# Kernel tuning notes

Measured on AMD Instinct MI355X. Metric: run time of the kernel, lower is better.

Reference implementation:

```python
import jax, jax.numpy as jnp
import numpy as np

N, D_IN, D_OUT, E, K = 32768, 1024, 1024, 8, 2
LN_EPS = 1e-5


def setup_inputs() -> dict:
    key = jax.random.key(0)
    ks = jax.random.split(key, 7)
    x = jax.random.normal(ks[0], (N, D_IN), dtype=jnp.float32)
    # gate: Linear(D_IN, E) then Tanh
    Wg = jax.random.normal(ks[1], (D_IN, E), dtype=jnp.float32) * 0.02
    bg = jnp.zeros((E,), dtype=jnp.float32)
    # experts: stacked Linear(D_IN, D_OUT) weights, [E, D_IN, D_OUT]
    We = jax.random.normal(ks[2], (E, D_IN, D_OUT), dtype=jnp.float32) * 0.02
    be = jnp.zeros((E, D_OUT), dtype=jnp.float32)
    # per-expert LayerNorm params
    gamma = jnp.ones((E, D_OUT), dtype=jnp.float32)
    beta = jnp.zeros((E, D_OUT), dtype=jnp.float32)
    return {"x": x, "Wg": Wg, "bg": bg, "We": We, "be": be,
            "gamma": gamma, "beta": beta}


def reference(x, Wg, bg, We, be, gamma, beta):
    # gating: Linear + Tanh, then top-k over experts, softmax over the k gates
    gate_logits = jnp.tanh(x @ Wg + bg)                      # [N, E]
    top_g, top_i = jax.lax.top_k(gate_logits, K)             # [N, K], [N, K]
    gates = jax.nn.softmax(top_g, axis=-1)                   # [N, K]

    # all experts computed densely (faithful to original): Linear + GELU + LN
    h = jnp.einsum('ni,eio->neo', x, We) + be[None]          # [N, E, D_OUT]
    h = jax.nn.gelu(h, approximate=False)                    # torch nn.GELU (exact)
    mu = jnp.mean(h, axis=-1, keepdims=True)
    var = jnp.mean(jnp.square(h - mu), axis=-1, keepdims=True)
    h = (h - mu) * jax.lax.rsqrt(var + LN_EPS)
    h = h * gamma[None] + beta[None]                         # [N, E, D_OUT]

    # gather top-k expert outputs and combine with softmax gates
    sel = jnp.take_along_axis(h, top_i[:, :, None], axis=1)  # [N, K, D_OUT]
    return jnp.sum(sel * gates[:, :, None], axis=1)          # [N, D_OUT]
```

## Files before the change

kernel.cpp:

```cpp
#include <hip/hip_runtime.h>
#include <hip/hip_bf16.h>

#define N_TOK 32768
#define D_IN 1024
#define D_OUT 1024
#define NE 8

#define BM 128
#define BN 128
#define BK 64
#define PAD 72

#define GBLK 64
#define GCH 64
#define NCH (D_IN / GCH)
#define CNT_STRIDE 64

#define AS1 __attribute__((address_space(1)))
#define AS3 __attribute__((address_space(3)))

typedef __attribute__((ext_vector_type(8))) short short8;
typedef __attribute__((ext_vector_type(4))) float floatx4;

__device__ __forceinline__ unsigned short f2bf(float f) {
    union { float f; unsigned u; } v; v.f = f;
    unsigned r = v.u + 0x7fffu + ((v.u >> 16) & 1u);
    return (unsigned short)(r >> 16);
}
__device__ __forceinline__ float bf2f(unsigned short u) {
    union { unsigned u; float f; } v; v.u = ((unsigned)u) << 16;
    return v.f;
}

__device__ __forceinline__ void gl_lds16(const void* g, void* l) {
    __builtin_amdgcn_global_load_lds((const AS1 unsigned int*)g,
                                     (AS3 unsigned int*)l, 16, 0, 0);
}

__global__ void zero_cnt(int* __restrict__ cnt) {
    int i = blockIdx.x * 256 + threadIdx.x;
    if (i < 16 * CNT_STRIDE) cnt[i] = 0;
}

__global__ __launch_bounds__(256) void transpose_we(
    const float* __restrict__ We, unsigned short* __restrict__ WeT)
{
    __shared__ unsigned short tile[64 * 65];
    int e = blockIdx.z;
    int i0 = blockIdx.x * 64, o0 = blockIdx.y * 64;
    const float* src = We + ((size_t)e * D_IN + i0) * D_OUT + o0;
#pragma unroll
    for (int it = 0; it < 16; ++it) {
        int idx = threadIdx.x + it * 256;
        int r = idx >> 6, c = idx & 63;
        tile[r * 65 + c] = f2bf(src[(size_t)r * D_OUT + c]);
    }
    __syncthreads();
    unsigned short* dst = WeT + ((size_t)e * D_OUT + o0) * D_IN + i0;
#pragma unroll
    for (int it = 0; it < 16; ++it) {
        int idx = threadIdx.x + it * 256;
        int r = idx >> 6, c = idx & 63;
        dst[(size_t)r * D_IN + c] = tile[c * 65 + r];
    }
}

__global__ __launch_bounds__(256) void gate_kernel(
    const float* __restrict__ x, const float* __restrict__ Wg,
    const float* __restrict__ bg,
    int* __restrict__ top_i, float* __restrict__ gates,
    int* __restrict__ cnt, int* __restrict__ lists,
    unsigned short* __restrict__ xb)
{
    __shared__ float xs[GBLK][GCH + 1];
    __shared__ float wgs[4][136];
    __shared__ int lcnt[16];
    __shared__ int lbase[16];
    __shared__ int ltoks[16][GBLK];

    int tid = threadIdx.x;
    if (tid < 16) lcnt[tid] = 0;

    int tok0 = blockIdx.x * GBLK;
    int lane = tid & 63, wave = tid >> 6;
    int t = lane >> 2, q = lane & 3;
    int row = wave * 16 + t;
    int token = tok0 + row;

    double acc[NE] = {};

#pragma unroll 1
    for (int c = 0; c < NCH; ++c) {
        int cb = c * GCH;
        __syncthreads();
        {
            int i = tid;
#pragma unroll
            for (int it = 0; it < 2; ++it, i += 256) {
                float v = Wg[(size_t)cb * NE + i];
                int d = i >> 3, e = i & 7;
                wgs[d >> 4][(d & 15) * 8 + e] = v;
            }
        }
#pragma unroll
        for (int it = 0; it < 4; ++it) {
            int idx = tid + it * 256;
            int r = idx >> 4, c4 = (idx & 15) * 4;
            const float4 v = *(const float4*)(x + (size_t)(tok0 + r) * D_IN + cb + c4);
            xs[r][c4 + 0] = v.x; xs[r][c4 + 1] = v.y;
            xs[r][c4 + 2] = v.z; xs[r][c4 + 3] = v.w;
            ushort4 pk;
            pk.x = f2bf(v.x); pk.y = f2bf(v.y); pk.z = f2bf(v.z); pk.w = f2bf(v.w);
            *(ushort4*)(xb + (size_t)(tok0 + r) * D_IN + cb + c4) = pk;
        }
        __syncthreads();
#pragma unroll
        for (int jj = 0; jj < 16; ++jj) {
            double xd = (double)xs[row][q * 16 + jj];
            const float* wr = &wgs[q][jj * 8];
#pragma unroll
            for (int e = 0; e < NE; ++e)
                acc[e] += xd * (double)wr[e];
        }
    }

#pragma unroll
    for (int off = 1; off <= 2; off <<= 1)
#pragma unroll
        for (int e = 0; e < NE; ++e)
            acc[e] += __shfl_xor(acc[e], off, 64);

    float lg[NE];
#pragma unroll
    for (int e = 0; e < NE; ++e) lg[e] = tanhf((float)(acc[e] + (double)bg[e]));
    int i0 = 0;
    for (int e = 1; e < NE; ++e) if (lg[e] > lg[i0]) i0 = e;
    int i1 = (i0 == 0) ? 1 : 0;
    for (int e = 0; e < NE; ++e) { if (e == i0) continue; if (lg[e] > lg[i1]) i1 = e; }
    float tt = expf(lg[i1] - lg[i0]);
    float g0 = 1.0f / (1.0f + tt);
    float g1 = tt * g0;

    if (q == 0) {
        top_i[token * 2 + 0] = i0; top_i[token * 2 + 1] = i1;
        gates[token * 2 + 0] = g0; gates[token * 2 + 1] = g1;
        int p0 = atomicAdd(&lcnt[i0], 1);
        ltoks[i0][p0] = token;
        int p1 = atomicAdd(&lcnt[NE + i1], 1);
        ltoks[NE + i1][p1] = token;
    }
    __syncthreads();
    if (tid < 16) lbase[tid] = atomicAdd(&cnt[tid * CNT_STRIDE], lcnt[tid]);
    __syncthreads();
    int g = tid >> 4, j = tid & 15;
    int n = lcnt[g];
    int* dst = lists + (size_t)g * N_TOK + lbase[g];
    for (int k = j; k < n; k += 16) dst[k] = ltoks[g][k];
}

__global__ __launch_bounds__(256) void gemm_slot2(
    const unsigned short* __restrict__ xb,
    const unsigned short* __restrict__ WeT,
    const float* __restrict__ be, const int* __restrict__ lists,
    const int* __restrict__ cnt, int zoff,
    unsigned short* __restrict__ h0, unsigned short* __restrict__ h1)
{
    int z = blockIdx.z + zoff;
    int slot = z >> 3, e = z & 7;
    unsigned short* __restrict__ h = slot ? h1 : h0;
    int count = cnt[z * CNT_STRIDE];
    int mact = (count + BM - 1) >> 7;
    int o = blockIdx.x + 8 * blockIdx.y;
    int xcd = o & 7, idx = o >> 3;
    if (idx >= mact) return;
    int wk = xcd * mact + idx;
    int m0 = (wk >> 3) * BM;
    int n0 = (wk & 7) * BN;
    const int* list = lists + (size_t)z * N_TOK;

    __shared__ int toks[BM];
    __shared__ __align__(16) unsigned short As[BM * BK];
    __shared__ __align__(16) unsigned short Bs[BN * BK];

    int tid = threadIdx.x;
    if (tid < BM) {
        int r = m0 + tid; if (r > count - 1) r = count - 1;
        toks[tid] = list[r];
    }
    __syncthreads();

    int lane = tid & 63, wave = tid >> 6;
    int wm = (wave & 1) * 64, wn = (wave >> 1) * 64;
    int q = lane & 15, quad = lane >> 4;

    const unsigned short* Bglob = WeT + ((size_t)e * D_OUT + n0) * D_IN;

    const unsigned short* asrc[4];
    const unsigned short* bsrc[4];
    unsigned short* adst[4];
    unsigned short* bdst[4];
#pragma unroll
    for (int it = 0; it < 4; ++it) {
        int idx2 = tid + it * 256;
        int m = idx2 >> 3, c = idx2 & 7;
        int sc = c ^ (m & 7);
        asrc[it] = xb + (size_t)toks[m] * D_IN + sc * 8;
        bsrc[it] = Bglob + (size_t)m * D_IN + sc * 8;
        adst[it] = As + (size_t)(it * 256 + (tid & 192)) * 8;
        bdst[it] = Bs + (size_t)(it * 256 + (tid & 192)) * 8;
    }

    floatx4 acc[4][4] = {};

    for (int kb = 0; kb < D_IN; kb += BK) {
#pragma unroll
        for (int it = 0; it < 4; ++it)
            gl_lds16(asrc[it] + kb, adst[it]);
#pragma unroll
        for (int it = 0; it < 4; ++it)
            gl_lds16(bsrc[it] + kb, bdst[it]);
        __syncthreads();

#pragma unroll
        for (int ks = 0; ks < BK; ks += 32) {
            int cb = ks >> 3;
            short8 af[4], bfr[4];
#pragma unroll
            for (int i = 0; i < 4; ++i) {
                int row = wm + i * 16 + q;
                int ch = (cb + quad) ^ (row & 7);
                af[i] = *(const short8*)&As[row * BK + ch * 8];
            }
#pragma unroll
            for (int j = 0; j < 4; ++j) {
                int row = wn + j * 16 + q;
                int ch = (cb + quad) ^ (row & 7);
                bfr[j] = *(const short8*)&Bs[row * BK + ch * 8];
            }
#pragma unroll
            for (int i = 0; i < 4; ++i)
#pragma unroll
                for (int j = 0; j < 4; ++j)
                    acc[i][j] = __builtin_amdgcn_mfma_f32_16x16x32_bf16(
                        af[i], bfr[j], acc[i][j], 0, 0, 0);
        }
        __syncthreads();
    }

#pragma unroll
    for (int i = 0; i < 4; ++i) {
#pragma unroll
        for (int r = 0; r < 4; ++r) {
            int m = wm + i * 16 + quad * 4 + r;
            if (m0 + m < count) {
                int tok = toks[m];
#pragma unroll
                for (int j = 0; j < 4; ++j) {
                    int n = n0 + wn + j * 16 + q;
                    float v = acc[i][j][r] + be[(size_t)e * D_OUT + n];
                    h[(size_t)tok * D_OUT + n] = f2bf(v);
                }
            }
        }
    }
}

__global__ __launch_bounds__(256) void gemm_slot_f32(
    const float* __restrict__ x,
    const unsigned short* __restrict__ WeT,
    const float* __restrict__ be, const int* __restrict__ lists,
    const int* __restrict__ cnt, int slot, unsigned short* __restrict__ h)
{
    int e = blockIdx.z;
    int count = cnt[(slot * NE + e) * CNT_STRIDE];
    int m0 = blockIdx.y * BM;
    if (m0 >= count) return;
    int n0 = blockIdx.x * BN;
    const int* list = lists + (size_t)(slot * NE + e) * N_TOK;

    __shared__ int toks[BM];
    __shared__ unsigned short As[BM * PAD];
    __shared__ unsigned short Bs[BN * PAD];

    int tid = threadIdx.x;
    if (tid < BM) {
        int r = m0 + tid; if (r > count - 1) r = count - 1;
        toks[tid] = list[r];
    }
    __syncthreads();

    int lane = tid & 63, wave = tid >> 6;
    int wm = (wave & 1) * 64, wn = (wave >> 1) * 64;
    int q = lane & 15, quad = lane >> 4;

    floatx4 acc[4][4] = {};
    const unsigned short* Bglob = WeT + ((size_t)e * D_OUT + n0) * D_IN;

    for (int kb = 0; kb < D_IN; kb += BK) {
#pragma unroll
        for (int it = 0; it < 8; ++it) {
            int idx = tid + it * 256;
            int m = idx >> 4, kq = idx & 15;
            float4 v = *(const float4*)(x + (size_t)toks[m] * D_IN + kb + kq * 4);
            ushort4 pk;
            pk.x = f2bf(v.x); pk.y = f2bf(v.y); pk.z = f2bf(v.z); pk.w = f2bf(v.w);
            *(ushort4*)&As[m * PAD + kq * 4] = pk;
        }
#pragma unroll
        for (int it = 0; it < 4; ++it) {
            int idx = tid + it * 256;
            int n = idx >> 3, kq = idx & 7;
            *(uint4*)&Bs[n * PAD + kq * 8] =
                *(const uint4*)(Bglob + (size_t)n * D_IN + kb + kq * 8);
        }
        __syncthreads();
#pragma unroll
        for (int ks = 0; ks < BK; ks += 32) {
            short8 af[4], bfr[4];
#pragma unroll
            for (int i = 0; i < 4; ++i)
                af[i] = *(const short8*)&As[(wm + i * 16 + q) * PAD + ks + quad * 8];
#pragma unroll
            for (int j = 0; j < 4; ++j)
                bfr[j] = *(const short8*)&Bs[(wn + j * 16 + q) * PAD + ks + quad * 8];
#pragma unroll
            for (int i = 0; i < 4; ++i)
#pragma unroll
                for (int j = 0; j < 4; ++j)
                    acc[i][j] = __builtin_amdgcn_mfma_f32_16x16x32_bf16(
                        af[i], bfr[j], acc[i][j], 0, 0, 0);
        }
        __syncthreads();
    }

#pragma unroll
    for (int i = 0; i < 4; ++i) {
#pragma unroll
        for (int r = 0; r < 4; ++r) {
            int m = wm + i * 16 + quad * 4 + r;
            if (m0 + m < count) {
                int tok = toks[m];
#pragma unroll
                for (int j = 0; j < 4; ++j) {
                    int n = n0 + wn + j * 16 + q;
                    float v = acc[i][j][r] + be[(size_t)e * D_OUT + n];
                    h[(size_t)tok * D_OUT + n] = f2bf(v);
                }
            }
        }
    }
}

__global__ __launch_bounds__(256) void ln_combine(
    const unsigned short* __restrict__ h, const float* __restrict__ gamma,
    const float* __restrict__ beta, const float* __restrict__ gates,
    const int* __restrict__ top_i, int slot, float* __restrict__ out)
{
    int wave = threadIdx.x >> 6, lane = threadIdx.x & 63;
    int token = blockIdx.x * 4 + wave;
    int e = top_i[token * 2 + slot];
    float gate = gates[token * 2 + slot];
    const unsigned short* hr = h + (size_t)token * D_OUT;

    float g[16], sum = 0.f, sumsq = 0.f;
#pragma unroll
    for (int jj = 0; jj < 4; ++jj) {
        int n = jj * 256 + lane * 4;
        uint2 pk = *(const uint2*)(hr + n);
        float v0 = bf2f((unsigned short)(pk.x & 0xffff));
        float v1 = bf2f((unsigned short)(pk.x >> 16));
        float v2 = bf2f((unsigned short)(pk.y & 0xffff));
        float v3 = bf2f((unsigned short)(pk.y >> 16));
        float g0 = 0.5f * v0 * (1.0f + erff(v0 * 0.70710678118654752f));
        float g1 = 0.5f * v1 * (1.0f + erff(v1 * 0.70710678118654752f));
        float g2 = 0.5f * v2 * (1.0f + erff(v2 * 0.70710678118654752f));
        float g3 = 0.5f * v3 * (1.0f + erff(v3 * 0.70710678118654752f));
        g[jj * 4 + 0] = g0; g[jj * 4 + 1] = g1; g[jj * 4 + 2] = g2; g[jj * 4 + 3] = g3;
        sum   += g0 + g1 + g2 + g3;
        sumsq += g0 * g0 + g1 * g1 + g2 * g2 + g3 * g3;
    }
#pragma unroll
    for (int off = 32; off; off >>= 1) {
        sum   += __shfl_xor(sum, off, 64);
        sumsq += __shfl_xor(sumsq, off, 64);
    }
    float mu  = sum * (1.0f / 1024.0f);
    float var = sumsq * (1.0f / 1024.0f) - mu * mu;
    float rs  = rsqrtf(var + 1e-5f);

    const float* gm = gamma + (size_t)e * D_OUT;
    const float* bt = beta  + (size_t)e * D_OUT;
    float* orow = out + (size_t)token * D_OUT;
#pragma unroll
    for (int jj = 0; jj < 4; ++jj) {
        int n = jj * 256 + lane * 4;
        float4 gm4 = *(const float4*)(gm + n);
        float4 bt4 = *(const float4*)(bt + n);
        float4 o;
        o.x = gate * ((g[jj * 4 + 0] - mu) * rs * gm4.x + bt4.x);
        o.y = gate * ((g[jj * 4 + 1] - mu) * rs * gm4.y + bt4.y);
        o.z = gate * ((g[jj * 4 + 2] - mu) * rs * gm4.z + bt4.z);
        o.w = gate * ((g[jj * 4 + 3] - mu) * rs * gm4.w + bt4.w);
        if (slot == 0) {
            *(float4*)(orow + n) = o;
        } else {
            float4 p = *(const float4*)(orow + n);
            p.x += o.x; p.y += o.y; p.z += o.z; p.w += o.w;
            *(float4*)(orow + n) = p;
        }
    }
}

__global__ __launch_bounds__(256) void ln_combine2(
    const unsigned short* __restrict__ h0, const unsigned short* __restrict__ h1,
    const float* __restrict__ gamma, const float* __restrict__ beta,
    const float* __restrict__ gates, const int* __restrict__ top_i,
    float* __restrict__ out)
{
    int wave = threadIdx.x >> 6, lane = threadIdx.x & 63;
    int token = blockIdx.x * 4 + wave;
    int e0 = top_i[token * 2 + 0], e1 = top_i[token * 2 + 1];
    float gate0 = gates[token * 2 + 0], gate1 = gates[token * 2 + 1];

    float g[2][16], mu[2], rs[2];
    const unsigned short* hr[2] = { h0 + (size_t)token * D_OUT,
                                    h1 + (size_t)token * D_OUT };
#pragma unroll
    for (int s = 0; s < 2; ++s) {
        float sum = 0.f, sumsq = 0.f;
#pragma unroll
        for (int jj = 0; jj < 4; ++jj) {
            int n = jj * 256 + lane * 4;
            uint2 pk = *(const uint2*)(hr[s] + n);
            float v0 = bf2f((unsigned short)(pk.x & 0xffff));
            float v1 = bf2f((unsigned short)(pk.x >> 16));
            float v2 = bf2f((unsigned short)(pk.y & 0xffff));
            float v3 = bf2f((unsigned short)(pk.y >> 16));
            float a0 = 0.5f * v0 * (1.0f + erff(v0 * 0.70710678118654752f));
            float a1 = 0.5f * v1 * (1.0f + erff(v1 * 0.70710678118654752f));
            float a2 = 0.5f * v2 * (1.0f + erff(v2 * 0.70710678118654752f));
            float a3 = 0.5f * v3 * (1.0f + erff(v3 * 0.70710678118654752f));
            g[s][jj * 4 + 0] = a0; g[s][jj * 4 + 1] = a1;
            g[s][jj * 4 + 2] = a2; g[s][jj * 4 + 3] = a3;
            sum   += a0 + a1 + a2 + a3;
            sumsq += a0 * a0 + a1 * a1 + a2 * a2 + a3 * a3;
        }
#pragma unroll
        for (int off = 32; off; off >>= 1) {
            sum   += __shfl_xor(sum, off, 64);
            sumsq += __shfl_xor(sumsq, off, 64);
        }
        float m = sum * (1.0f / 1024.0f);
        float var = sumsq * (1.0f / 1024.0f) - m * m;
        mu[s] = m;
        rs[s] = rsqrtf(var + 1e-5f);
    }

    const float* gm0 = gamma + (size_t)e0 * D_OUT;
    const float* bt0 = beta  + (size_t)e0 * D_OUT;
    const float* gm1 = gamma + (size_t)e1 * D_OUT;
    const float* bt1 = beta  + (size_t)e1 * D_OUT;
    float* orow = out + (size_t)token * D_OUT;
#pragma unroll
    for (int jj = 0; jj < 4; ++jj) {
        int n = jj * 256 + lane * 4;
        float4 gmA = *(const float4*)(gm0 + n);
        float4 btA = *(const float4*)(bt0 + n);
        float4 gmB = *(const float4*)(gm1 + n);
        float4 btB = *(const float4*)(bt1 + n);
        float4 o;
        o.x = gate0 * ((g[0][jj * 4 + 0] - mu[0]) * rs[0] * gmA.x + btA.x)
            + gate1 * ((g[1][jj * 4 + 0] - mu[1]) * rs[1] * gmB.x + btB.x);
        o.y = gate0 * ((g[0][jj * 4 + 1] - mu[0]) * rs[0] * gmA.y + btA.y)
            + gate1 * ((g[1][jj * 4 + 1] - mu[1]) * rs[1] * gmB.y + btB.y);
        o.z = gate0 * ((g[0][jj * 4 + 2] - mu[0]) * rs[0] * gmA.z + btA.z)
            + gate1 * ((g[1][jj * 4 + 2] - mu[1]) * rs[1] * gmB.z + btB.z);
        o.w = gate0 * ((g[0][jj * 4 + 3] - mu[0]) * rs[0] * gmA.w + btA.w)
            + gate1 * ((g[1][jj * 4 + 3] - mu[1]) * rs[1] * gmB.w + btB.w);
        *(float4*)(orow + n) = o;
    }
}

extern "C" void kernel_launch(void* const* d_in, const int* in_sizes, int n_in,
                              void* d_out, int out_size, void* d_ws, size_t ws_size,
                              hipStream_t stream) {
    const float* x     = (const float*)d_in[0];
    const float* Wg    = (const float*)d_in[1];
    const float* bg    = (const float*)d_in[2];
    const float* We    = (const float*)d_in[3];
    const float* be    = (const float*)d_in[4];
    const float* gamma = (const float*)d_in[5];
    const float* beta  = (const float*)d_in[6];
    float* out = (float*)d_out;

    char* w = (char*)d_ws;
    size_t off = 0;
    int*   cnt   = (int*)(w + off);            off += (size_t)16 * CNT_STRIDE * 4;
    int*   top_i = (int*)(w + off);            off += (size_t)N_TOK * 2 * 4;
    float* gates = (float*)(w + off);          off += (size_t)N_TOK * 2 * 4;
    int*   lists = (int*)(w + off);            off += (size_t)16 * N_TOK * 4;
    unsigned short* WeT = (unsigned short*)(w + off); off += (size_t)NE * D_IN * D_OUT * 2;
    unsigned short* h   = (unsigned short*)(w + off); off += (size_t)N_TOK * D_OUT * 2;
    size_t xb_bytes = (size_t)N_TOK * D_IN * 2;
    bool use_bf = (off + xb_bytes) <= ws_size;
    unsigned short* xb = use_bf ? (unsigned short*)(w + off) : h;
    if (use_bf) off += xb_bytes;
    size_t h1_bytes = (size_t)N_TOK * D_OUT * 2;
    bool use_fused = use_bf && (off + h1_bytes) <= ws_size;
    unsigned short* h1 = use_fused ? (unsigned short*)(w + off) : h;
    if (use_fused) off += h1_bytes;

    zero_cnt<<<(16 * CNT_STRIDE + 255) / 256, 256, 0, stream>>>(cnt);
    transpose_we<<<dim3(16, 16, NE), 256, 0, stream>>>(We, WeT);
    gate_kernel<<<N_TOK / GBLK, 256, 0, stream>>>(x, Wg, bg, top_i, gates, cnt, lists, xb);

    if (use_fused) {
        gemm_slot2<<<dim3(D_OUT / BN, N_TOK / BM, 16), 256, 0, stream>>>(
            xb, WeT, be, lists, cnt, 0, h, h1);
        ln_combine2<<<N_TOK / 4, 256, 0, stream>>>(h, h1, gamma, beta, gates, top_i, out);
    } else if (use_bf) {
        for (int s = 0; s < 2; ++s) {
            gemm_slot2<<<dim3(D_OUT / BN, N_TOK / BM, 8), 256, 0, stream>>>(
                xb, WeT, be, lists, cnt, s * 8, h, h);
            ln_combine<<<N_TOK / 4, 256, 0, stream>>>(h, gamma, beta, gates, top_i, s, out);
        }
    } else {
        for (int s = 0; s < 2; ++s) {
            gemm_slot_f32<<<dim3(D_OUT / BN, N_TOK / BM, 8), 256, 0, stream>>>(
                x, WeT, be, lists, cnt, s, h);
            ln_combine<<<N_TOK / 4, 256, 0, stream>>>(h, gamma, beta, gates, top_i, s, out);
        }
    }
}
```

Before: 555.1 us.

## Double-buffer LDS tiles in expert GEMM and shrink gate block size

The expert GEMM now keeps two LDS buffers for the A and B tiles. It issues the global-to-LDS loads for the next K tile before running the MFMAs on the current one, so memory latency overlaps with compute, and it uses a single barrier per step instead of two. The gate kernel drops to 32 tokens per block with 8 lanes per token, which doubles the number of gate blocks for more parallelism and adds one more shuffle-reduction round. Double buffering doubles LDS use (about 64KB), which may lower occupancy. Overlap may also be limited because the wait on vmcnt(0) sits right after compute.

```diff
diff --git a/kernel.cpp b/kernel.cpp
--- a/kernel.cpp
+++ b/kernel.cpp
@@ -11,7 +11,7 @@
 #define BK 64
 #define PAD 72
 
-#define GBLK 64
+#define GBLK 32
 #define GCH 64
 #define NCH (D_IN / GCH)
 #define CNT_STRIDE 64
@@ -73,7 +73,7 @@
     unsigned short* __restrict__ xb)
 {
     __shared__ float xs[GBLK][GCH + 1];
-    __shared__ float wgs[4][136];
+    __shared__ float wgs[8][68];
     __shared__ int lcnt[16];
     __shared__ int lbase[16];
     __shared__ int ltoks[16][GBLK];
@@ -83,8 +83,8 @@
 
     int tok0 = blockIdx.x * GBLK;
     int lane = tid & 63, wave = tid >> 6;
-    int t = lane >> 2, q = lane & 3;
-    int row = wave * 16 + t;
+    int t = lane >> 3, q = lane & 7;
+    int row = wave * 8 + t;
     int token = tok0 + row;
 
     double acc[NE] = {};
@@ -94,16 +94,16 @@
         int cb = c * GCH;
         __syncthreads();
         {
-            int i = tid;
-#pragma unroll
-            for (int it = 0; it < 2; ++it, i += 256) {
+#pragma unroll
+            for (int it = 0; it < 2; ++it) {
+                int i = tid + it * 256;
                 float v = Wg[(size_t)cb * NE + i];
                 int d = i >> 3, e = i & 7;
-                wgs[d >> 4][(d & 15) * 8 + e] = v;
+                wgs[d >> 3][(d & 7) * 8 + e] = v;
             }
         }
 #pragma unroll
-        for (int it = 0; it < 4; ++it) {
+        for (int it = 0; it < 2; ++it) {
             int idx = tid + it * 256;
             int r = idx >> 4, c4 = (idx & 15) * 4;
             const float4 v = *(const float4*)(x + (size_t)(tok0 + r) * D_IN + cb + c4);
@@ -115,8 +115,8 @@
         }
         __syncthreads();
 #pragma unroll
-        for (int jj = 0; jj < 16; ++jj) {
-            double xd = (double)xs[row][q * 16 + jj];
+        for (int jj = 0; jj < 8; ++jj) {
+            double xd = (double)xs[row][q * 8 + jj];
             const float* wr = &wgs[q][jj * 8];
 #pragma unroll
             for (int e = 0; e < NE; ++e)
@@ -125,7 +125,7 @@
     }
 
 #pragma unroll
-    for (int off = 1; off <= 2; off <<= 1)
+    for (int off = 1; off <= 4; off <<= 1)
 #pragma unroll
         for (int e = 0; e < NE; ++e)
             acc[e] += __shfl_xor(acc[e], off, 64);
@@ -179,8 +179,8 @@
     const int* list = lists + (size_t)z * N_TOK;
 
     __shared__ int toks[BM];
-    __shared__ __align__(16) unsigned short As[BM * BK];
-    __shared__ __align__(16) unsigned short Bs[BN * BK];
+    __shared__ __align__(16) unsigned short As[2][BM * BK];
+    __shared__ __align__(16) unsigned short Bs[2][BN * BK];
 
     int tid = threadIdx.x;
     if (tid < BM) {
@@ -197,8 +197,7 @@
 
     const unsigned short* asrc[4];
     const unsigned short* bsrc[4];
-    unsigned short* adst[4];
-    unsigned short* bdst[4];
+    int ldsoff[4];
 #pragma unroll
     for (int it = 0; it < 4; ++it) {
         int idx2 = tid + it * 256;
@@ -206,36 +205,49 @@
         int sc = c ^ (m & 7);
         asrc[it] = xb + (size_t)toks[m] * D_IN + sc * 8;
         bsrc[it] = Bglob + (size_t)m * D_IN + sc * 8;
-        adst[it] = As + (size_t)(it * 256 + (tid & 192)) * 8;
-        bdst[it] = Bs + (size_t)(it * 256 + (tid & 192)) * 8;
+        ldsoff[it] = (it * 256 + (tid & 192)) * 8;
     }
 
     floatx4 acc[4][4] = {};
 
-    for (int kb = 0; kb < D_IN; kb += BK) {
-#pragma unroll
-        for (int it = 0; it < 4; ++it)
-            gl_lds16(asrc[it] + kb, adst[it]);
-#pragma unroll
-        for (int it = 0; it < 4; ++it)
-            gl_lds16(bsrc[it] + kb, bdst[it]);
-        __syncthreads();
-
+#pragma unroll
+    for (int it = 0; it < 4; ++it) gl_lds16(asrc[it], &As[0][ldsoff[it]]);
+#pragma unroll
+    for (int it = 0; it < 4; ++it) gl_lds16(bsrc[it], &Bs[0][ldsoff[it]]);
+    asm volatile("s_waitcnt vmcnt(0)" ::: "memory");
+    __builtin_amdgcn_s_barrier();
+    asm volatile("" ::: "memory");
+
+    const int NT = D_IN / BK;
+    int cur = 0;
+#pragma unroll 1
+    for (int tstep = 0; tstep < NT; ++tstep) {
+        if (tstep + 1 < NT) {
+            int kb = (tstep + 1) * BK;
+            unsigned short* Ad = &As[cur ^ 1][0];
+            unsigned short* Bd = &Bs[cur ^ 1][0];
+#pragma unroll
+            for (int it = 0; it < 4; ++it) gl_lds16(asrc[it] + kb, Ad + ldsoff[it]);
+#pragma unroll
+            for (int it = 0; it < 4; ++it) gl_lds16(bsrc[it] + kb, Bd + ldsoff[it]);
+        }
+        const unsigned short* Ab = &As[cur][0];
+        const unsigned short* Bb = &Bs[cur][0];
 #pragma unroll
         for (int ks = 0; ks < BK; ks += 32) {
             int cb = ks >> 3;
             short8 af[4], bfr[4];
 #pragma unroll
             for (int i = 0; i < 4; ++i) {
-                int row = wm + i * 16 + q;
-                int ch = (cb + quad) ^ (row & 7);
-                af[i] = *(const short8*)&As[row * BK + ch * 8];
+                int rw = wm + i * 16 + q;
+                int ch = (cb + quad) ^ (rw & 7);
+                af[i] = *(const short8*)&Ab[rw * BK + ch * 8];
             }
 #pragma unroll
             for (int j = 0; j < 4; ++j) {
-                int row = wn + j * 16 + q;
-                int ch = (cb + quad) ^ (row & 7);
-                bfr[j] = *(const short8*)&Bs[row * BK + ch * 8];
+                int rw = wn + j * 16 + q;
+                int ch = (cb + quad) ^ (rw & 7);
+                bfr[j] = *(const short8*)&Bb[rw * BK + ch * 8];
             }
 #pragma unroll
             for (int i = 0; i < 4; ++i)
@@ -244,7 +256,12 @@
                     acc[i][j] = __builtin_amdgcn_mfma_f32_16x16x32_bf16(
                         af[i], bfr[j], acc[i][j], 0, 0, 0);
         }
-        __syncthreads();
+        if (tstep + 1 < NT) {
+            asm volatile("s_waitcnt vmcnt(0)" ::: "memory");
+            __builtin_amdgcn_s_barrier();
+            asm volatile("" ::: "memory");
+            cur ^= 1;
+        }
     }
 
 #pragma unroll
```

New measurement: 563.7 us. No clear change (+1.5%).
